# Kernel optimization log

Hardware: AMD Instinct MI355X
Metric: run time of the kernel (lower is better)

The kernel has to match this reference:

```python
import jax, jax.numpy as jnp
import numpy as np

D_MODEL = 1024
NHEAD = 16
HEAD_DIM = D_MODEL // NHEAD


def setup_inputs() -> dict:
    key = jax.random.key(0)
    ks = jax.random.split(key, 6)
    scale = 0.02
    x = jax.random.normal(ks[0], (8, 1024, D_MODEL), dtype=jnp.float32)
    # nn.Linear weights are [out, in]; per-head q/k/v stacked over heads
    W_split = jax.random.normal(ks[1], (D_MODEL, D_MODEL), dtype=jnp.float32) * scale
    W_out = jax.random.normal(ks[2], (D_MODEL, D_MODEL), dtype=jnp.float32) * scale
    Wq = jax.random.normal(ks[3], (NHEAD, HEAD_DIM, HEAD_DIM), dtype=jnp.float32) * scale
    Wk = jax.random.normal(ks[4], (NHEAD, HEAD_DIM, HEAD_DIM), dtype=jnp.float32) * scale
    Wv = jax.random.normal(ks[5], (NHEAD, HEAD_DIM, HEAD_DIM), dtype=jnp.float32) * scale
    return {"x": x, "W_split": W_split, "W_out": W_out, "Wq": Wq, "Wk": Wk, "Wv": Wv}


def reference(x, W_split, W_out, Wq, Wk, Wv):
    b, s, _ = x.shape
    # x_proj: [b, s, h, hd]
    xp = (x @ W_split.T).reshape(b, s, NHEAD, HEAD_DIM)
    # per-head Linear (weight [out,in]): y = x @ W.T
    q = jnp.einsum('bshd,hod->bsho', xp, Wq)
    k = jnp.einsum('bshd,hod->bsho', xp, Wk)
    v = jnp.einsum('bshd,hod->bsho', xp, Wv)
    # scores scaled by sqrt(head_dim) (Attention.d_model == head_dim)
    scores = jnp.einsum('bsho,btho->bhst', q, k) / jnp.sqrt(jnp.float32(HEAD_DIM))
    attn = jax.nn.softmax(scores, axis=-1)  # [b, h, s, s]
    out = jnp.einsum('bhst,btho->bsho', attn, v)  # [b, s, h, hd]
    concat = out.reshape(b, s, D_MODEL)
    return concat @ W_out.T
```

## Files before the change

kernel.cpp:

```cpp
#include <hip/hip_runtime.h>
#include <math.h>

#define NHEAD 16
#define HD 64
#define DMODEL 1024
#define SEQ 1024
#define BATCH 8
#define ROWS (BATCH * SEQ)

typedef __attribute__((ext_vector_type(8))) short bf16x8;
typedef __attribute__((ext_vector_type(8))) short short8v;
typedef __attribute__((ext_vector_type(4))) float f32x4;
typedef __attribute__((ext_vector_type(16))) float f32x16;
typedef __attribute__((ext_vector_type(4))) short short4v;
typedef __attribute__((ext_vector_type(4))) unsigned int uint32x4;

__device__ __forceinline__ unsigned short f2bf(float f) {
    unsigned u = __builtin_bit_cast(unsigned, f);
    u += 0x7FFF + ((u >> 16) & 1);
    return (unsigned short)(u >> 16);
}

__device__ __forceinline__ float fexp2(float x) {
#if __has_builtin(__builtin_amdgcn_exp2f)
    return __builtin_amdgcn_exp2f(x);
#else
    return __expf(x * 0.6931471805599453f);
#endif
}

__device__ __forceinline__ void gload16(const void* g, void* l) {
    __builtin_amdgcn_global_load_lds(
        (const __attribute__((address_space(1))) unsigned int*)g,
        (__attribute__((address_space(3))) unsigned int*)l, 16, 0, 0);
}

#define QSCALE 0.18033688011112042f
__global__ __launch_bounds__(256) void cvt_all(const float* __restrict__ x,
                                               const float* __restrict__ Ws,
                                               const float* __restrict__ Wo,
                                               const float* __restrict__ Wq,
                                               const float* __restrict__ Wk,
                                               const float* __restrict__ Wv,
                                               unsigned short* __restrict__ xb,
                                               unsigned short* __restrict__ wsb,
                                               unsigned short* __restrict__ wob,
                                               unsigned short* __restrict__ wqb,
                                               unsigned short* __restrict__ wkb,
                                               unsigned short* __restrict__ wvb) {
    int bid = blockIdx.x;
    const float* src; unsigned short* dst; float scale = 1.f;
    if (bid < 4096)      { src = x;  dst = xb;  }
    else if (bid < 4608) { src = Ws; dst = wsb; bid -= 4096; }
    else if (bid < 5120) { src = Wo; dst = wob; bid -= 4608; }
    else if (bid < 5152) { src = Wq; dst = wqb; bid -= 5120; scale = QSCALE; }
    else if (bid < 5184) { src = Wk; dst = wkb; bid -= 5152; }
    else                 { src = Wv; dst = wvb; bid -= 5184; }
    int i = (bid * 256 + threadIdx.x) * 8;
    float4 a = *(const float4*)(src + i);
    float4 b = *(const float4*)(src + i + 4);
    short8v o;
    o[0] = (short)f2bf(a.x * scale); o[1] = (short)f2bf(a.y * scale);
    o[2] = (short)f2bf(a.z * scale); o[3] = (short)f2bf(a.w * scale);
    o[4] = (short)f2bf(b.x * scale); o[5] = (short)f2bf(b.y * scale);
    o[6] = (short)f2bf(b.z * scale); o[7] = (short)f2bf(b.w * scale);
    *(short8v*)(dst + i) = o;
}

__global__ __launch_bounds__(512) void gemm1_qkv(const unsigned short* __restrict__ A,
                                                 const unsigned short* __restrict__ B,
                                                 const unsigned short* __restrict__ wqb,
                                                 const unsigned short* __restrict__ wkb,
                                                 const unsigned short* __restrict__ wvb,
                                                 unsigned short* __restrict__ qb,
                                                 unsigned short* __restrict__ kbuf,
                                                 unsigned short* __restrict__ vT) {
    __shared__ char lds[65536];
    const int tid  = threadIdx.x;
    const int w    = tid >> 6;
    const int lane = tid & 63;
    const int lr   = lane & 15, lg = lane >> 4;
    const int wr   = w >> 1,  wc = w & 1;
    const int m0   = blockIdx.x * 128;
    const int n0   = blockIdx.y * 128;
    const int K    = DMODEL;

    f32x4 acc[2][4] = {};

    const int srow   = lane >> 3;
    const int swbyte = ((lane & 7) ^ srow) << 4;

#define G1_STAGE(buf, k0)                                                          \
    {                                                                              \
        _Pragma("unroll")                                                          \
        for (int c = 0; c < 2; ++c) {                                              \
            int chunk = w * 2 + c;                                                 \
            int row   = chunk * 8 + srow;                                          \
            gload16((const char*)A + ((size_t)(m0 + row) * K + (k0)) * 2 + swbyte, \
                    lds + (buf) * 16384 + chunk * 1024);                           \
            gload16((const char*)B + ((size_t)(n0 + row) * K + (k0)) * 2 + swbyte, \
                    lds + 32768 + (buf) * 16384 + chunk * 1024);                   \
        }                                                                          \
    }

    G1_STAGE(0, 0);
    __syncthreads();

    int cur = 0;
    for (int t = 0; t < K / 64; ++t) {
        if (t + 1 < K / 64) G1_STAGE(cur ^ 1, (t + 1) * 64);

#pragma unroll
        for (int k2 = 0; k2 < 2; ++k2) {
            bf16x8 af[2], bg[4];
#pragma unroll
            for (int f = 0; f < 2; ++f) {
                int row = wr * 32 + f * 16 + lr;
                af[f] = *(const bf16x8*)(lds + cur * 16384 + row * 128 +
                                         ((k2 * 64 + lg * 16) ^ ((row & 7) << 4)));
            }
#pragma unroll
            for (int g = 0; g < 4; ++g) {
                int row = wc * 64 + g * 16 + lr;
                bg[g] = *(const bf16x8*)(lds + 32768 + cur * 16384 + row * 128 +
                                         ((k2 * 64 + lg * 16) ^ ((row & 7) << 4)));
            }
#pragma unroll
            for (int f = 0; f < 2; ++f)
#pragma unroll
                for (int g = 0; g < 4; ++g)
                    acc[f][g] = __builtin_amdgcn_mfma_f32_16x16x32_bf16(af[f], bg[g],
                                                                        acc[f][g], 0, 0, 0);
        }
        __syncthreads();
        cur ^= 1;
    }
#undef G1_STAGE

#pragma unroll
    for (int f = 0; f < 2; ++f)
#pragma unroll
        for (int g = 0; g < 4; ++g)
#pragma unroll
            for (int r = 0; r < 4; ++r) {
                int mrow = wr * 32 + f * 16 + lg * 4 + r;
                int ncol = wc * 64 + g * 16 + lr;
                *(unsigned short*)(lds + mrow * 256 + ((ncol * 2) ^ ((mrow & 7) << 4))) =
                    f2bf(acc[f][g][r]);
            }

    const int b  = m0 >> 10;
    const int sl = m0 & 1023;

#pragma unroll
    for (int hh = 0; hh < 2; ++hh) {
        const int h = blockIdx.y * 2 + hh;
#pragma unroll
        for (int i = 0; i < 3; ++i) {
            int c   = w * 3 + i;
            int p   = c >> 3, rc = c & 7;
            int row = rc * 8 + srow;
            const unsigned short* ws = (p == 0) ? wqb : (p == 1) ? wkb : wvb;
            gload16((const char*)ws + ((size_t)(h * 64 + row) * 64) * 2 + swbyte,
                    lds + 32768 + p * 8192 + rc * 1024);
        }
        __syncthreads();

        f32x4 a2[3][4] = {};
#pragma unroll
        for (int k2 = 0; k2 < 2; ++k2) {
            int arow = w * 16 + lr;
            bf16x8 af = *(const bf16x8*)(lds + arow * 256 +
                                         ((hh * 128 + k2 * 64 + lg * 16) ^ ((arow & 7) << 4)));
#pragma unroll
            for (int p = 0; p < 3; ++p)
#pragma unroll
                for (int g = 0; g < 4; ++g) {
                    int o = g * 16 + lr;
                    bf16x8 bg = *(const bf16x8*)(lds + 32768 + p * 8192 + o * 128 +
                                                 ((k2 * 64 + lg * 16) ^ ((o & 7) << 4)));
                    a2[p][g] = __builtin_amdgcn_mfma_f32_16x16x32_bf16(af, bg,
                                                                       a2[p][g], 0, 0, 0);
                }
        }

#pragma unroll
        for (int g = 0; g < 4; ++g) {
#pragma unroll
            for (int r = 0; r < 4; ++r) {
                size_t idx = (size_t)(m0 + w * 16 + lg * 4 + r) * DMODEL +
                             h * 64 + g * 16 + lr;
                qb[idx]   = f2bf(a2[0][g][r]);
                kbuf[idx] = f2bf(a2[1][g][r]);
            }
            short4v pv;
#pragma unroll
            for (int r = 0; r < 4; ++r) pv[r] = (short)f2bf(a2[2][g][r]);
            size_t o = (size_t)(b * 16 + h) * 64 + g * 16 + lr;
            *(short4v*)(vT + o * SEQ + sl + w * 16 + lg * 4) = pv;
        }
        __syncthreads();
    }
}

__global__ __launch_bounds__(512) void gemm_bf16(const unsigned short* __restrict__ A,
                                                 const unsigned short* __restrict__ B,
                                                 float* __restrict__ Cf,
                                                 int M, int N, int K) {
    __shared__ char sA[2][16384];
    __shared__ char sB[2][16384];
    const int tid  = threadIdx.x;
    const int w    = tid >> 6;
    const int lane = tid & 63;
    const int lr   = lane & 15, lg = lane >> 4;
    const int wr   = w >> 1,  wc = w & 1;
    const int m0   = blockIdx.x * 128;
    const int n0   = blockIdx.y * 128;

    f32x4 acc[2][4] = {};

    const int srow   = lane >> 3;
    const int swbyte = ((lane & 7) ^ srow) << 4;
    const int nt     = K / 64;

#define GEMM_STAGE(buf, k0)                                                        \
    {                                                                              \
        _Pragma("unroll")                                                          \
        for (int c = 0; c < 2; ++c) {                                              \
            int chunk = w * 2 + c;                                                 \
            int row   = chunk * 8 + srow;                                          \
            gload16((const char*)A + ((size_t)(m0 + row) * K + (k0)) * 2 + swbyte, \
                    sA[buf] + chunk * 1024);                                       \
            gload16((const char*)B + ((size_t)(n0 + row) * K + (k0)) * 2 + swbyte, \
                    sB[buf] + chunk * 1024);                                       \
        }                                                                          \
    }

    GEMM_STAGE(0, 0);
    __syncthreads();

    int cur = 0;
    for (int t = 0; t < nt; ++t) {
        if (t + 1 < nt) GEMM_STAGE(cur ^ 1, (t + 1) * 64);

#pragma unroll
        for (int k2 = 0; k2 < 2; ++k2) {
            bf16x8 af[2], bg[4];
#pragma unroll
            for (int f = 0; f < 2; ++f) {
                int row = wr * 32 + f * 16 + lr;
                af[f] = *(const bf16x8*)(sA[cur] + row * 128 +
                                         ((k2 * 64 + lg * 16) ^ ((row & 7) << 4)));
            }
#pragma unroll
            for (int g = 0; g < 4; ++g) {
                int row = wc * 64 + g * 16 + lr;
                bg[g] = *(const bf16x8*)(sB[cur] + row * 128 +
                                         ((k2 * 64 + lg * 16) ^ ((row & 7) << 4)));
            }
#pragma unroll
            for (int f = 0; f < 2; ++f)
#pragma unroll
                for (int g = 0; g < 4; ++g)
                    acc[f][g] = __builtin_amdgcn_mfma_f32_16x16x32_bf16(af[f], bg[g],
                                                                        acc[f][g], 0, 0, 0);
        }
        __syncthreads();
        cur ^= 1;
    }
#undef GEMM_STAGE

#pragma unroll
    for (int f = 0; f < 2; ++f)
#pragma unroll
        for (int g = 0; g < 4; ++g)
#pragma unroll
            for (int r = 0; r < 4; ++r)
                Cf[(size_t)(m0 + wr * 32 + f * 16 + lg * 4 + r) * N +
                   n0 + wc * 64 + g * 16 + lr] = acc[f][g][r];
}

__global__ __launch_bounds__(512) void attn_mfma(const unsigned short* __restrict__ qb,
                                                 const unsigned short* __restrict__ kb,
                                                 const unsigned short* __restrict__ vT,
                                                 unsigned short* __restrict__ ob) {
    __shared__ unsigned short sK[4][4096];
    __shared__ unsigned short sV[4][4096];

    const int tid  = threadIdx.x;
    const int w    = tid >> 6;
    const int lane = tid & 63;
    const int ql   = lane & 31;
    const int hl   = lane >> 5;
    const int bh   = blockIdx.x;
    const int b    = bh >> 4, h = bh & 15;
    const int s0   = blockIdx.y * 256;
    const int NT   = SEQ / 64;

    const unsigned short* qrow = qb + ((size_t)(b * SEQ + s0 + w * 32 + ql) * DMODEL + h * 64);
    bf16x8 qf[4];
#pragma unroll
    for (int s = 0; s < 4; ++s)
        qf[s] = *(const bf16x8*)(qrow + 16 * s + 8 * hl);

    f32x16 acc0 = {}, acc1 = {};
    float l0 = 0.f, l1 = 0.f, l2 = 0.f, l3 = 0.f;

    const int srow = lane >> 3;
    const int ssw  = ((lane & 7) << 4) ^ (srow << 4);
    const int swz  = (ql & 7) << 4;
    int byos[4];
#pragma unroll
    for (int s = 0; s < 4; ++s) byos[s] = (32 * s + 16 * hl) ^ swz;

#define ATTN_STAGE(buf, kt)                                                          \
    {                                                                                \
        int row = w * 8 + srow;                                                      \
        gload16((const char*)kb +                                                    \
                    (((size_t)(b * SEQ + (kt) * 64 + row) * DMODEL + h * 64) * 2) + ssw, \
                (char*)sK[buf] + w * 1024);                                          \
        gload16((const char*)vT +                                                    \
                    (((size_t)(bh * 64 + row) * SEQ + (kt) * 64) * 2) + ssw,         \
                (char*)sV[buf] + w * 1024);                                          \
    }

    ATTN_STAGE(0, 0);
    ATTN_STAGE(1, 1);
    asm volatile("s_waitcnt vmcnt(2)" ::: "memory");
    __builtin_amdgcn_s_barrier();
    __builtin_amdgcn_sched_barrier(0);

    for (int kt = 0; kt < NT; ++kt) {
        const int cb = kt & 3;
        if (kt + 2 < NT) ATTN_STAGE((kt + 2) & 3, kt + 2);

        f32x16 st0 = {}, st1 = {};
        __builtin_amdgcn_s_setprio(1);
#pragma unroll
        for (int s = 0; s < 4; ++s) {
            bf16x8 kf0 = *(const bf16x8*)((const char*)sK[cb] + ql * 128 + byos[s]);
            bf16x8 kf1 = *(const bf16x8*)((const char*)sK[cb] + (32 + ql) * 128 + byos[s]);
            st0 = __builtin_amdgcn_mfma_f32_32x32x16_bf16(kf0, qf[s], st0, 0, 0, 0);
            st1 = __builtin_amdgcn_mfma_f32_32x32x16_bf16(kf1, qf[s], st1, 0, 0, 0);
        }
        __builtin_amdgcn_s_setprio(0);

        bf16x8 pf[4];
#define TILE_P(stv, PF0, PF1)                                                       \
        {                                                                           \
            float p_[16];                                                           \
            _Pragma("unroll")                                                       \
            for (int i = 0; i < 16; ++i) p_[i] = fexp2(stv[i]);                     \
            _Pragma("unroll")                                                       \
            for (int i = 0; i < 4; ++i) {                                           \
                l0 += p_[4 * i];     l1 += p_[4 * i + 1];                           \
                l2 += p_[4 * i + 2]; l3 += p_[4 * i + 3];                           \
            }                                                                       \
            unsigned pk_[8];                                                        \
            _Pragma("unroll")                                                       \
            for (int i = 0; i < 8; ++i)                                             \
                asm("v_cvt_pk_bf16_f32 %0, %1, %2"                                  \
                    : "=v"(pk_[i]) : "v"(p_[2 * i]), "v"(p_[2 * i + 1]));           \
            auto rA = __builtin_amdgcn_permlane32_swap(pk_[0], pk_[2], false, false); \
            auto rB = __builtin_amdgcn_permlane32_swap(pk_[1], pk_[3], false, false); \
            auto rC = __builtin_amdgcn_permlane32_swap(pk_[4], pk_[6], false, false); \
            auto rD = __builtin_amdgcn_permlane32_swap(pk_[5], pk_[7], false, false); \
            uint32x4 f0, f1;                                                        \
            f0[0] = rA[0]; f0[1] = rB[0]; f0[2] = rA[1]; f0[3] = rB[1];             \
            f1[0] = rC[0]; f1[1] = rD[0]; f1[2] = rC[1]; f1[3] = rD[1];             \
            PF0 = __builtin_bit_cast(bf16x8, f0);                                   \
            PF1 = __builtin_bit_cast(bf16x8, f1);                                   \
        }
        TILE_P(st0, pf[0], pf[1]);
        TILE_P(st1, pf[2], pf[3]);
#undef TILE_P

        __builtin_amdgcn_s_setprio(1);
#pragma unroll
        for (int s = 0; s < 4; ++s) {
            bf16x8 vf0 = *(const bf16x8*)((const char*)sV[cb] + ql * 128 + byos[s]);
            bf16x8 vf1 = *(const bf16x8*)((const char*)sV[cb] + (32 + ql) * 128 + byos[s]);
            acc0 = __builtin_amdgcn_mfma_f32_32x32x16_bf16(vf0, pf[s], acc0, 0, 0, 0);
            acc1 = __builtin_amdgcn_mfma_f32_32x32x16_bf16(vf1, pf[s], acc1, 0, 0, 0);
        }
        __builtin_amdgcn_s_setprio(0);

        if (kt + 2 < NT) { asm volatile("s_waitcnt vmcnt(2)" ::: "memory"); }
        else             { asm volatile("s_waitcnt vmcnt(0)" ::: "memory"); }
        __builtin_amdgcn_s_barrier();
        __builtin_amdgcn_sched_barrier(0);
    }
#undef ATTN_STAGE

    float l_ = (l0 + l1) + (l2 + l3);
    float lf = l_ + __shfl_xor(l_, 32, 64);
    float inv = 1.f / lf;
    const size_t rowbase = (size_t)(b * SEQ + s0 + w * 32 + ql) * DMODEL + h * 64;
#pragma unroll
    for (int g = 0; g < 4; ++g) {
        short4v o0, o1;
#pragma unroll
        for (int r = 0; r < 4; ++r) {
            o0[r] = (short)f2bf(acc0[4 * g + r] * inv);
            o1[r] = (short)f2bf(acc1[4 * g + r] * inv);
        }
        int d = 8 * g + 4 * hl;
        *(short4v*)(ob + rowbase + d)      = o0;
        *(short4v*)(ob + rowbase + 32 + d) = o1;
    }
}

extern "C" void kernel_launch(void* const* d_in, const int* in_sizes, int n_in,
                              void* d_out, int out_size, void* d_ws, size_t ws_size,
                              hipStream_t stream) {
    const float* x       = (const float*)d_in[0];
    const float* W_split = (const float*)d_in[1];
    const float* W_out   = (const float*)d_in[2];
    const float* Wq      = (const float*)d_in[3];
    const float* Wk      = (const float*)d_in[4];
    const float* Wv      = (const float*)d_in[5];
    float* out = (float*)d_out;

    unsigned short* xb  = (unsigned short*)d_ws;
    unsigned short* obb = xb;
    unsigned short* wsb = xb + (size_t)ROWS * DMODEL;
    unsigned short* wob = wsb + (size_t)DMODEL * DMODEL;
    unsigned short* qbuf= wob + (size_t)DMODEL * DMODEL;
    unsigned short* kbuf= qbuf + (size_t)ROWS * DMODEL;
    unsigned short* vT  = kbuf + (size_t)ROWS * DMODEL;
    unsigned short* wqb = vT + (size_t)ROWS * DMODEL;
    unsigned short* wkb = wqb + (size_t)NHEAD * HD * HD;
    unsigned short* wvb = wkb + (size_t)NHEAD * HD * HD;

    cvt_all<<<dim3(5216), dim3(256), 0, stream>>>(x, W_split, W_out, Wq, Wk, Wv,
                                                  xb, wsb, wob, wqb, wkb, wvb);
    gemm1_qkv<<<dim3(ROWS / 128, DMODEL / 128), dim3(512), 0, stream>>>(
        xb, wsb, wqb, wkb, wvb, qbuf, kbuf, vT);
    attn_mfma<<<dim3(BATCH * NHEAD, SEQ / 256), dim3(512), 0, stream>>>(qbuf, kbuf, vT, obb);
    gemm_bf16<<<dim3(ROWS / 128, DMODEL / 128), dim3(512), 0, stream>>>(
        obb, wob, out, ROWS, DMODEL, DMODEL);
}
```

Measured before the change: 113.1 us.

## Process attention K/V tiles in pairs and preload both heads' projection weights

The attention loop now handles two 64-key tiles per iteration with one barrier, double-buffering pairs of tiles in the four LDS slots and waiting on all outstanding loads before each barrier. This replaces the previous one-tile-per-iteration loop with a partial vmcnt wait. In the QKV GEMM, the per-head Wq/Wk/Wv weights for both heads are loaded into a larger LDS buffer up front, which drops a sync per head. The costs are more LDS in the GEMM, which may reduce occupancy, and a full vmcnt(0) wait that may expose load latency.

```diff
diff --git a/kernel.cpp b/kernel.cpp
--- a/kernel.cpp
+++ b/kernel.cpp
@@ -75,7 +75,7 @@
                                                  unsigned short* __restrict__ qb,
                                                  unsigned short* __restrict__ kbuf,
                                                  unsigned short* __restrict__ vT) {
-    __shared__ char lds[65536];
+    __shared__ char lds[81920];
     const int tid  = threadIdx.x;
     const int w    = tid >> 6;
     const int lane = tid & 63;
@@ -149,23 +149,27 @@
                     f2bf(acc[f][g][r]);
             }
 
+#pragma unroll
+    for (int i = 0; i < 6; ++i) {
+        int c   = w * 6 + i;
+        int p   = c >> 3;
+        int rc  = c & 7;
+        int row = rc * 8 + srow;
+        int hh  = p >= 3;
+        int pj  = p - 3 * hh;
+        int h   = blockIdx.y * 2 + hh;
+        const unsigned short* ws = (pj == 0) ? wqb : (pj == 1) ? wkb : wvb;
+        gload16((const char*)ws + ((size_t)(h * 64 + row) * 64) * 2 + swbyte,
+                lds + 32768 + p * 8192 + rc * 1024);
+    }
+    __syncthreads();
+
     const int b  = m0 >> 10;
     const int sl = m0 & 1023;
 
 #pragma unroll
     for (int hh = 0; hh < 2; ++hh) {
         const int h = blockIdx.y * 2 + hh;
-#pragma unroll
-        for (int i = 0; i < 3; ++i) {
-            int c   = w * 3 + i;
-            int p   = c >> 3, rc = c & 7;
-            int row = rc * 8 + srow;
-            const unsigned short* ws = (p == 0) ? wqb : (p == 1) ? wkb : wvb;
-            gload16((const char*)ws + ((size_t)(h * 64 + row) * 64) * 2 + swbyte,
-                    lds + 32768 + p * 8192 + rc * 1024);
-        }
-        __syncthreads();
-
         f32x4 a2[3][4] = {};
 #pragma unroll
         for (int k2 = 0; k2 < 2; ++k2) {
@@ -177,7 +181,7 @@
 #pragma unroll
                 for (int g = 0; g < 4; ++g) {
                     int o = g * 16 + lr;
-                    bf16x8 bg = *(const bf16x8*)(lds + 32768 + p * 8192 + o * 128 +
+                    bf16x8 bg = *(const bf16x8*)(lds + 32768 + (hh * 3 + p) * 8192 + o * 128 +
                                                  ((k2 * 64 + lg * 16) ^ ((o & 7) << 4)));
                     a2[p][g] = __builtin_amdgcn_mfma_f32_16x16x32_bf16(af, bg,
                                                                        a2[p][g], 0, 0, 0);
@@ -199,7 +203,6 @@
             size_t o = (size_t)(b * 16 + h) * 64 + g * 16 + lr;
             *(short4v*)(vT + o * SEQ + sl + w * 16 + lg * 4) = pv;
         }
-        __syncthreads();
     }
 }
 
@@ -295,7 +298,7 @@
     const int bh   = blockIdx.x;
     const int b    = bh >> 4, h = bh & 15;
     const int s0   = blockIdx.y * 256;
-    const int NT   = SEQ / 64;
+    const int NP   = SEQ / 128;
 
     const unsigned short* qrow = qb + ((size_t)(b * SEQ + s0 + w * 32 + ql) * DMODEL + h * 64);
     bf16x8 qf[4];
@@ -324,28 +327,6 @@
                 (char*)sV[buf] + w * 1024);                                          \
     }
 
-    ATTN_STAGE(0, 0);
-    ATTN_STAGE(1, 1);
-    asm volatile("s_waitcnt vmcnt(2)" ::: "memory");
-    __builtin_amdgcn_s_barrier();
-    __builtin_amdgcn_sched_barrier(0);
-
-    for (int kt = 0; kt < NT; ++kt) {
-        const int cb = kt & 3;
-        if (kt + 2 < NT) ATTN_STAGE((kt + 2) & 3, kt + 2);
-
-        f32x16 st0 = {}, st1 = {};
-        __builtin_amdgcn_s_setprio(1);
-#pragma unroll
-        for (int s = 0; s < 4; ++s) {
-            bf16x8 kf0 = *(const bf16x8*)((const char*)sK[cb] + ql * 128 + byos[s]);
-            bf16x8 kf1 = *(const bf16x8*)((const char*)sK[cb] + (32 + ql) * 128 + byos[s]);
-            st0 = __builtin_amdgcn_mfma_f32_32x32x16_bf16(kf0, qf[s], st0, 0, 0, 0);
-            st1 = __builtin_amdgcn_mfma_f32_32x32x16_bf16(kf1, qf[s], st1, 0, 0, 0);
-        }
-        __builtin_amdgcn_s_setprio(0);
-
-        bf16x8 pf[4];
 #define TILE_P(stv, PF0, PF1)                                                       \
         {                                                                           \
             float p_[16];                                                           \
@@ -371,25 +352,57 @@
             PF0 = __builtin_bit_cast(bf16x8, f0);                                   \
             PF1 = __builtin_bit_cast(bf16x8, f1);                                   \
         }
-        TILE_P(st0, pf[0], pf[1]);
-        TILE_P(st1, pf[2], pf[3]);
-#undef TILE_P
-
-        __builtin_amdgcn_s_setprio(1);
-#pragma unroll
-        for (int s = 0; s < 4; ++s) {
-            bf16x8 vf0 = *(const bf16x8*)((const char*)sV[cb] + ql * 128 + byos[s]);
-            bf16x8 vf1 = *(const bf16x8*)((const char*)sV[cb] + (32 + ql) * 128 + byos[s]);
-            acc0 = __builtin_amdgcn_mfma_f32_32x32x16_bf16(vf0, pf[s], acc0, 0, 0, 0);
-            acc1 = __builtin_amdgcn_mfma_f32_32x32x16_bf16(vf1, pf[s], acc1, 0, 0, 0);
-        }
-        __builtin_amdgcn_s_setprio(0);
-
-        if (kt + 2 < NT) { asm volatile("s_waitcnt vmcnt(2)" ::: "memory"); }
-        else             { asm volatile("s_waitcnt vmcnt(0)" ::: "memory"); }
+
+#define ATTN_TILE(cb)                                                               \
+    {                                                                               \
+        f32x16 st0 = {}, st1 = {};                                                  \
+        __builtin_amdgcn_s_setprio(1);                                              \
+        _Pragma("unroll")                                                           \
+        for (int s = 0; s < 4; ++s) {                                               \
+            bf16x8 kf0 = *(const bf16x8*)((const char*)sK[cb] + ql * 128 + byos[s]);\
+            bf16x8 kf1 = *(const bf16x8*)((const char*)sK[cb] + (32 + ql) * 128 + byos[s]); \
+            st0 = __builtin_amdgcn_mfma_f32_32x32x16_bf16(kf0, qf[s], st0, 0, 0, 0);\
+            st1 = __builtin_amdgcn_mfma_f32_32x32x16_bf16(kf1, qf[s], st1, 0, 0, 0);\
+        }                                                                           \
+        __builtin_amdgcn_s_setprio(0);                                              \
+        bf16x8 pf[4];                                                               \
+        TILE_P(st0, pf[0], pf[1]);                                                  \
+        TILE_P(st1, pf[2], pf[3]);                                                  \
+        __builtin_amdgcn_s_setprio(1);                                              \
+        _Pragma("unroll")                                                           \
+        for (int s = 0; s < 4; ++s) {                                               \
+            bf16x8 vf0 = *(const bf16x8*)((const char*)sV[cb] + ql * 128 + byos[s]);\
+            bf16x8 vf1 = *(const bf16x8*)((const char*)sV[cb] + (32 + ql) * 128 + byos[s]); \
+            acc0 = __builtin_amdgcn_mfma_f32_32x32x16_bf16(vf0, pf[s], acc0, 0, 0, 0); \
+            acc1 = __builtin_amdgcn_mfma_f32_32x32x16_bf16(vf1, pf[s], acc1, 0, 0, 0); \
+        }                                                                           \
+        __builtin_amdgcn_s_setprio(0);                                              \
+    }
+
+    ATTN_STAGE(0, 0);
+    ATTN_STAGE(1, 1);
+    asm volatile("s_waitcnt vmcnt(0)" ::: "memory");
+    __builtin_amdgcn_s_barrier();
+    __builtin_amdgcn_sched_barrier(0);
+
+    for (int P = 0; P < NP; ++P) {
+        const int slot = (P & 1) << 1;
+        if (P + 1 < NP) {
+            ATTN_STAGE(slot ^ 2, 2 * (P + 1));
+            ATTN_STAGE((slot ^ 2) + 1, 2 * (P + 1) + 1);
+        }
+        __builtin_amdgcn_sched_barrier(0);
+
+        ATTN_TILE(slot);
+        __builtin_amdgcn_sched_barrier(0);
+        ATTN_TILE(slot + 1);
+
+        asm volatile("s_waitcnt vmcnt(0)" ::: "memory");
         __builtin_amdgcn_s_barrier();
         __builtin_amdgcn_sched_barrier(0);
     }
+#undef ATTN_TILE
+#undef TILE_P
 #undef ATTN_STAGE
 
     float l_ = (l0 + l1) + (l2 + l3);
```

New measurement: 117.1 us. +3.6%, slower.
